# Kernel optimization log

Hardware: AMD Instinct MI355X
Metric: run time of the kernel (lower is better)

The kernel has to match this reference:

```python
import jax, jax.numpy as jnp
import numpy as np

X_DIM = 512
Z_DIM = 16
HEADS = 8
DIM_HEAD = 64
INNER = HEADS * DIM_HEAD
EPS = 1e-5


def _layernorm(t, g, b):
    mu = jnp.mean(t, axis=-1, keepdims=True)
    var = jnp.mean(jnp.square(t - mu), axis=-1, keepdims=True)
    return (t - mu) * jax.lax.rsqrt(var + EPS) * g + b


def setup_inputs() -> dict:
    key = jax.random.key(0)
    ks = jax.random.split(key, 8)
    B, N = 4, 2048
    s_x = 1.0 / np.sqrt(X_DIM)
    s_z = 1.0 / np.sqrt(Z_DIM)
    s_i = 1.0 / np.sqrt(INNER)
    return {
        "x": jax.random.normal(ks[0], (B, N, X_DIM), dtype=jnp.float32),
        "z": jax.random.normal(ks[1], (B, 1, Z_DIM), dtype=jnp.float32),
        "ln_x_g": jnp.ones((X_DIM,), jnp.float32),
        "ln_x_b": jnp.zeros((X_DIM,), jnp.float32),
        "ln_z_g": jnp.ones((Z_DIM,), jnp.float32),
        "ln_z_b": jnp.zeros((Z_DIM,), jnp.float32),
        "Wq": jax.random.normal(ks[2], (X_DIM, INNER), jnp.float32) * s_x,
        "Wk": jax.random.normal(ks[3], (X_DIM, INNER), jnp.float32) * s_x,
        "Wv": jax.random.normal(ks[4], (X_DIM, INNER), jnp.float32) * s_x,
        "Wz": jax.random.normal(ks[5], (Z_DIM, 2 * X_DIM), jnp.float32) * s_z,
        "Wo": jax.random.normal(ks[6], (INNER, X_DIM), jnp.float32) * s_i,
        "bo": jnp.zeros((X_DIM,), jnp.float32),
    }


def reference(x, z, ln_x_g, ln_x_b, ln_z_g, ln_z_b, Wq, Wk, Wv, Wz, Wo, bo):
    scale = DIM_HEAD ** (-0.5)
    # z path: LN -> Linear -> SiLU -> split into FiLM scale/shift
    zp = jax.nn.silu(_layernorm(z, ln_z_g, ln_z_b) @ Wz)  # [B, 1, 2*x_dim]
    z1, z2 = jnp.split(zp, 2, axis=-1)
    x_mod = _layernorm(x, ln_x_g, ln_x_b) * z1 + z2       # [B, N, x_dim]
    B, N, _ = x.shape

    def heads(t):  # [B, N, inner] -> [B, h, N, d]
        return t.reshape(B, N, HEADS, DIM_HEAD).transpose(0, 2, 1, 3)

    q = heads(x_mod @ Wq)
    k = heads(x_mod @ Wk)
    v = heads(x_mod @ Wv)
    sim = jnp.einsum('bhid,bhjd->bhij', q, k) * scale
    attn = jax.nn.softmax(sim, axis=-1)
    out = jnp.einsum('bhij,bhjd->bhid', attn, v)           # [B, h, N, d]
    out = out.transpose(0, 2, 1, 3).reshape(B, N, INNER)
    return out @ Wo + bo
```

## Files before the change

kernel.cpp:

```cpp
#include <hip/hip_runtime.h>

#define XD 512
#define HEADS 8
#define DH 64
#define NSEQ 2048
#define NBATCH 4
#define NROWS (NBATCH*NSEQ)

#define SCALE_L2E 0.18033688011112042f
#define DEFER_THR 4.0f

typedef __attribute__((ext_vector_type(8))) short bf16x8;
typedef __attribute__((ext_vector_type(8))) unsigned short u16x8;
typedef __attribute__((ext_vector_type(4))) float f32x4;
typedef __attribute__((ext_vector_type(16))) float f32x16;

__device__ __forceinline__ unsigned short f2bf(float f) {
  union { float f; unsigned u; } v; v.f = f;
  return (unsigned short)((v.u + 0x7fffu + ((v.u >> 16) & 1u)) >> 16);
}

__device__ __forceinline__ float fexp2(float x) {
#if __has_builtin(__builtin_amdgcn_exp2f)
  return __builtin_amdgcn_exp2f(x);
#else
  return exp2f(x);
#endif
}

__device__ __forceinline__ unsigned cvt_pk_bf16(float lo, float hi) {
  unsigned r;
  asm("v_cvt_pk_bf16_f32 %0, %1, %2" : "=v"(r) : "v"(lo), "v"(hi));
  return r;
}

__device__ __forceinline__ void gload_lds16(const unsigned short* g, unsigned short* l) {
  __builtin_amdgcn_global_load_lds(
      (const __attribute__((address_space(1))) unsigned int*)g,
      (__attribute__((address_space(3))) unsigned int*)l, 16, 0, 0);
}

__global__ __launch_bounds__(256) void zpath_kernel(
    const float* __restrict__ z, const float* __restrict__ g, const float* __restrict__ b,
    const float* __restrict__ Wz, float* __restrict__ z12) {
  int bb = blockIdx.x;
  int t = threadIdx.x;
  float zv[16];
  float mean = 0.f;
#pragma unroll
  for (int i = 0; i < 16; ++i) { zv[i] = z[bb * 16 + i]; mean += zv[i]; }
  mean *= (1.f / 16.f);
  float var = 0.f;
#pragma unroll
  for (int i = 0; i < 16; ++i) { float d = zv[i] - mean; var += d * d; }
  var *= (1.f / 16.f);
  float rs = rsqrtf(var + 1e-5f);
  float zn[16];
#pragma unroll
  for (int i = 0; i < 16; ++i) zn[i] = (zv[i] - mean) * rs * g[i] + b[i];
  for (int c = t; c < 1024; c += 256) {
    float acc = 0.f;
#pragma unroll
    for (int i = 0; i < 16; ++i) acc += zn[i] * Wz[i * 1024 + c];
    float s = acc / (1.f + __expf(-acc));
    z12[bb * 1024 + c] = s;
  }
}

__global__ __launch_bounds__(256) void xmod_kernel(
    const float* __restrict__ x, const float* __restrict__ g, const float* __restrict__ b,
    const float* __restrict__ z12, unsigned short* __restrict__ xm) {
  int wave = threadIdx.x >> 6, lane = threadIdx.x & 63;
  int row = blockIdx.x * 4 + wave;
  const float* xr = x + (size_t)row * XD;
  float4 v0 = ((const float4*)xr)[lane * 2];
  float4 v1 = ((const float4*)xr)[lane * 2 + 1];
  float vv[8] = {v0.x, v0.y, v0.z, v0.w, v1.x, v1.y, v1.z, v1.w};
  float sum = 0.f, sq = 0.f;
#pragma unroll
  for (int i = 0; i < 8; ++i) { sum += vv[i]; sq += vv[i] * vv[i]; }
#pragma unroll
  for (int o = 32; o; o >>= 1) { sum += __shfl_xor(sum, o); sq += __shfl_xor(sq, o); }
  float mean = sum * (1.f / 512.f);
  float var = sq * (1.f / 512.f) - mean * mean;
  float rs = rsqrtf(var + 1e-5f);
  int bb = row >> 11;
  const float* zz = z12 + bb * 1024;
  int c0 = lane * 8;
  u16x8 o8;
#pragma unroll
  for (int i = 0; i < 8; ++i) {
    int c = c0 + i;
    float t = (vv[i] - mean) * rs * g[c] + b[c];
    t = t * zz[c] + zz[512 + c];
    o8[i] = f2bf(t);
  }
  *(u16x8*)(xm + (size_t)row * XD + c0) = o8;
}

__global__ __launch_bounds__(256) void wtrans4_kernel(
    const float* __restrict__ W0, const float* __restrict__ W1,
    const float* __restrict__ W2, const float* __restrict__ W3,
    unsigned short* __restrict__ dst) {
  int idx = blockIdx.x * 256 + threadIdx.x;
  int w = idx >> 18;
  int e = idx & 262143;
  int n = e >> 9, k = e & 511;
  const float* W = (w == 0) ? W0 : (w == 1) ? W1 : (w == 2) ? W2 : W3;
  dst[idx] = f2bf(W[k * 512 + n]);
}

__global__ __launch_bounds__(256, 2) void gemm_qkv_kernel(
    const unsigned short* __restrict__ A, const unsigned short* __restrict__ Wt,
    unsigned short* __restrict__ Qo, unsigned short* __restrict__ Ko,
    unsigned short* __restrict__ Vo) {
  __shared__ unsigned short Alds[128 * 64];
  __shared__ unsigned short Blds[128 * 64];
  int widx = threadIdx.x >> 6, lane = threadIdx.x & 63;
  int blk = blockIdx.x;
  int nt = blk % 12, mt = blk / 12;
  int blkM = mt * 128, blkN = nt * 128;
  int wr = widx >> 1, wc = widx & 1;
  int lr = lane & 15, lg = lane >> 4;
  int srow = lane >> 3, sc8 = lane & 7;

  f32x4 acc[4][4] = {};

  for (int kc = 0; kc < 512; kc += 64) {
#pragma unroll
    for (int i = 0; i < 4; ++i) {
      int rb = widx * 32 + i * 8;
      int row = rb + srow;
      int cs = (sc8 ^ (row & 7)) * 8;
      gload_lds16(A + (size_t)(blkM + row) * 512 + kc + cs, &Alds[rb * 64]);
      gload_lds16(Wt + (size_t)(blkN + row) * 512 + kc + cs, &Blds[rb * 64]);
    }
    __syncthreads();

#pragma unroll
    for (int kh = 0; kh < 2; ++kh) {
      bf16x8 bfr[4];
#pragma unroll
      for (int ni = 0; ni < 4; ++ni) {
        int brow = wc * 64 + ni * 16 + lr;
        bfr[ni] = *(const bf16x8*)&Blds[brow * 64 + (((kh * 4 + lg) ^ (brow & 7)) * 8)];
      }
#pragma unroll
      for (int mi = 0; mi < 4; ++mi) {
        int arow = wr * 64 + mi * 16 + lr;
        bf16x8 afr = *(const bf16x8*)&Alds[arow * 64 + (((kh * 4 + lg) ^ (arow & 7)) * 8)];
#pragma unroll
        for (int ni = 0; ni < 4; ++ni)
          acc[mi][ni] = __builtin_amdgcn_mfma_f32_16x16x32_bf16(afr, bfr[ni], acc[mi][ni], 0, 0, 0);
      }
    }
    __syncthreads();
  }

  int cg = blkN >> 9;
#pragma unroll
  for (int mi = 0; mi < 4; ++mi)
#pragma unroll
    for (int ni = 0; ni < 4; ++ni) {
      int col = blkN + wc * 64 + ni * 16 + lr;
      int c = col & 511;
#pragma unroll
      for (int j = 0; j < 4; ++j) {
        int row = blkM + wr * 64 + mi * 16 + lg * 4 + j;
        float v = acc[mi][ni][j];
        if (cg == 0) {
          Qo[(size_t)row * 512 + c] = f2bf(v * SCALE_L2E);
        } else if (cg == 1) {
          Ko[(size_t)row * 512 + c] = f2bf(v);
        } else {
          int bb = row >> 11, n = row & 2047, h = c >> 6, d = c & 63;
          int j4 = n & 15;
          int slot = (j4 & 3) | (((j4 >> 3) & 1) << 2) | (((j4 >> 2) & 1) << 3);
          int np = (n & ~15) | slot;
          Vo[(((size_t)(bb * HEADS + h) * DH + d) << 11) + np] = f2bf(v);
        }
      }
    }
}

__global__ __launch_bounds__(256, 2) void gemm_out_kernel(
    const unsigned short* __restrict__ A, const unsigned short* __restrict__ Wt,
    float* __restrict__ out, const float* __restrict__ bias) {
  __shared__ unsigned short Alds[128 * 64];
  __shared__ unsigned short Blds[64 * 64];
  int widx = threadIdx.x >> 6, lane = threadIdx.x & 63;
  int blk = blockIdx.x;
  int nt = blk & 7, mt = blk >> 3;
  int blkM = mt * 128, blkN = nt * 64;
  int wr = widx >> 1, wc = widx & 1;
  int lr = lane & 15, lg = lane >> 4;
  int srow = lane >> 3, sc8 = lane & 7;

  f32x4 acc[4][2] = {};

  for (int kc = 0; kc < 512; kc += 64) {
#pragma unroll
    for (int i = 0; i < 4; ++i) {
      int rb = widx * 32 + i * 8;
      int row = rb + srow;
      int cs = (sc8 ^ (row & 7)) * 8;
      gload_lds16(A + (size_t)(blkM + row) * 512 + kc + cs, &Alds[rb * 64]);
    }
#pragma unroll
    for (int i = 0; i < 2; ++i) {
      int rb = widx * 16 + i * 8;
      int row = rb + srow;
      int cs = (sc8 ^ (row & 7)) * 8;
      gload_lds16(Wt + (size_t)(blkN + row) * 512 + kc + cs, &Blds[rb * 64]);
    }
    __syncthreads();

#pragma unroll
    for (int kh = 0; kh < 2; ++kh) {
      bf16x8 bfr[2];
#pragma unroll
      for (int ni = 0; ni < 2; ++ni) {
        int brow = wc * 32 + ni * 16 + lr;
        bfr[ni] = *(const bf16x8*)&Blds[brow * 64 + (((kh * 4 + lg) ^ (brow & 7)) * 8)];
      }
#pragma unroll
      for (int mi = 0; mi < 4; ++mi) {
        int arow = wr * 64 + mi * 16 + lr;
        bf16x8 afr = *(const bf16x8*)&Alds[arow * 64 + (((kh * 4 + lg) ^ (arow & 7)) * 8)];
#pragma unroll
        for (int ni = 0; ni < 2; ++ni)
          acc[mi][ni] = __builtin_amdgcn_mfma_f32_16x16x32_bf16(afr, bfr[ni], acc[mi][ni], 0, 0, 0);
      }
    }
    __syncthreads();
  }

#pragma unroll
  for (int mi = 0; mi < 4; ++mi)
#pragma unroll
    for (int ni = 0; ni < 2; ++ni) {
      int col = blkN + wc * 32 + ni * 16 + lr;
#pragma unroll
      for (int j = 0; j < 4; ++j) {
        int row = blkM + wr * 64 + mi * 16 + lg * 4 + j;
        out[(size_t)row * 512 + col] = acc[mi][ni][j] + bias[col];
      }
    }
}


#define KVCHUNK 128
#define NCHUNK (NSEQ / KVCHUNK)

#define STAGE(buf, kcc) do {                                              \
    _Pragma("unroll")                                                     \
    for (int i = 0; i < 4; ++i) {                                         \
      int rbk = widx * 32 + i * 8;                                        \
      int rowk = rbk + (lane >> 3);                                       \
      int csk = (lane & 7) ^ (rowk & 7);                                  \
      gload_lds16(Kg + (size_t)((kcc) + rowk) * 512 + csk * 8, &Klds[buf][rbk * 64]); \
      int rbv = widx * 16 + i * 4;                                        \
      int rowv = rbv + (lane >> 4);                                       \
      int csv = (lane & 15) ^ (rowv & 15);                                \
      gload_lds16(Vg + (size_t)rowv * NSEQ + (kcc) + csv * 8, &Vlds[buf][rbv * 128]); \
    }                                                                     \
  } while (0)

#define PROCESS_LDS64(kb_, vb_, half) do {                                \
    f32x16 s[2];                                                          \
    __builtin_amdgcn_s_setprio(1);                                        \
    _Pragma("unroll")                                                     \
    for (int kt = 0; kt < 2; ++kt) {                                      \
      int krow = (half) * 64 + kt * 32 + ql;                              \
      f32x16 z = {};                                                      \
      _Pragma("unroll")                                                   \
      for (int ks = 0; ks < 4; ++ks) {                                    \
        bf16x8 kf = *(const bf16x8*)((kb_) + krow * 64 + (((ks * 2 + hi) ^ (krow & 7)) * 8)); \
        z = __builtin_amdgcn_mfma_f32_32x32x16_bf16(kf, qf[ks], z, 0, 0, 0); \
      }                                                                   \
      s[kt] = z;                                                          \
    }                                                                     \
    __builtin_amdgcn_s_setprio(0);                                        \
    float m8 = s[0][0];                                                   \
    _Pragma("unroll")                                                     \
    for (int i = 1; i < 16; ++i) m8 = fmaxf(m8, s[0][i]);                 \
    _Pragma("unroll")                                                     \
    for (int i = 0; i < 16; ++i) m8 = fmaxf(m8, s[1][i]);                 \
    m8 = fmaxf(m8, __shfl_xor(m8, 32));                                   \
    bool grow = (m8 > m0 + DEFER_THR);                                    \
    if (__any((int)grow)) {                                               \
      float mn = fmaxf(m0, m8);                                           \
      float al = fexp2(m0 - mn);                                          \
      m0 = mn; l0 *= al;                                                  \
      _Pragma("unroll")                                                   \
      for (int dt = 0; dt < 2; ++dt)                                      \
        _Pragma("unroll")                                                 \
        for (int j = 0; j < 16; ++j) o[dt][j] *= al;                      \
    }                                                                     \
    float p0[16], p1[16]; float rs = 0.f;                                 \
    _Pragma("unroll")                                                     \
    for (int i = 0; i < 16; ++i) { p0[i] = fexp2(s[0][i] - m0); rs += p0[i]; } \
    _Pragma("unroll")                                                     \
    for (int i = 0; i < 16; ++i) { p1[i] = fexp2(s[1][i] - m0); rs += p1[i]; } \
    rs += __shfl_xor(rs, 32);                                             \
    l0 += rs;                                                             \
    union { unsigned w[4]; bf16x8 v; } pf[4];                             \
    _Pragma("unroll")                                                     \
    for (int d2 = 0; d2 < 4; ++d2) {                                      \
      pf[0].w[d2] = cvt_pk_bf16(p0[2 * d2], p0[2 * d2 + 1]);              \
      pf[1].w[d2] = cvt_pk_bf16(p0[8 + 2 * d2], p0[8 + 2 * d2 + 1]);      \
      pf[2].w[d2] = cvt_pk_bf16(p1[2 * d2], p1[2 * d2 + 1]);              \
      pf[3].w[d2] = cvt_pk_bf16(p1[8 + 2 * d2], p1[8 + 2 * d2 + 1]);      \
    }                                                                     \
    __builtin_amdgcn_s_setprio(1);                                        \
    _Pragma("unroll")                                                     \
    for (int dt = 0; dt < 2; ++dt) {                                      \
      int vrow = dt * 32 + ql;                                            \
      f32x16 acc = o[dt];                                                 \
      _Pragma("unroll")                                                   \
      for (int g = 0; g < 4; ++g) {                                       \
        int sv = (half) * 8 + g * 2 + hi;                                 \
        bf16x8 vf = *(const bf16x8*)((vb_) + vrow * 128 + ((sv ^ (vrow & 15)) * 8)); \
        acc = __builtin_amdgcn_mfma_f32_32x32x16_bf16(vf, pf[g].v, acc, 0, 0, 0); \
      }                                                                   \
      o[dt] = acc;                                                        \
    }                                                                     \
    __builtin_amdgcn_s_setprio(0);                                        \
  } while (0)

__global__ __launch_bounds__(256, 2) void attn_kernel(
    const unsigned short* __restrict__ Q, const unsigned short* __restrict__ K,
    const unsigned short* __restrict__ VT, unsigned short* __restrict__ O) {
  __shared__ unsigned short Klds[2][128 * 64];
  __shared__ unsigned short Vlds[2][64 * 128];
  int widx = threadIdx.x >> 6, lane = threadIdx.x & 63;
  int blk = blockIdx.x;
  int xcd = blk & 7;
  int idx = blk >> 3;
  int bh = xcd * 4 + (idx >> 4);
  int qg = idx & 15;
  int b = bh >> 3, h = bh & 7;
  int ql = lane & 31, hi = lane >> 5;
  int qrow0 = qg * 128 + widx * 32;

  bf16x8 qf[4];
  const unsigned short* Qp = Q + (size_t)(b * NSEQ + qrow0 + ql) * 512 + h * 64 + hi * 8;
#pragma unroll
  for (int ks = 0; ks < 4; ++ks) qf[ks] = *(const bf16x8*)(Qp + ks * 16);

  const unsigned short* Kg = K + (size_t)b * NSEQ * 512 + h * 64;
  const unsigned short* Vg = VT + (size_t)bh * DH * NSEQ;

  float m0 = -3.0e38f, l0 = 0.f;
  f32x16 o[2] = {};

  STAGE(0, 0);
  __syncthreads();
  int cur = 0;
  for (int t = 0; t < NCHUNK; ++t) {
    if (t + 1 < NCHUNK) STAGE(cur ^ 1, (t + 1) * KVCHUNK);
    const unsigned short* kb_ = &Klds[cur][0];
    const unsigned short* vb_ = &Vlds[cur][0];
    PROCESS_LDS64(kb_, vb_, 0);
    PROCESS_LDS64(kb_, vb_, 1);
    __syncthreads();
    cur ^= 1;
  }

  {
    float inv = 1.f / l0;
    size_t rowb = (size_t)(b * NSEQ + qrow0 + ql) * 512 + h * 64 + hi * 4;
#pragma unroll
    for (int dt = 0; dt < 2; ++dt)
#pragma unroll
      for (int c = 0; c < 8; ++c) {
        unsigned w = cvt_pk_bf16(o[dt][2 * c] * inv, o[dt][2 * c + 1] * inv);
        int d0 = dt * 32 + 8 * (c >> 1) + (c & 1) * 2;
        *(unsigned*)(O + rowb + d0) = w;
      }
  }
}

extern "C" void kernel_launch(void* const* d_in, const int* in_sizes, int n_in,
                              void* d_out, int out_size, void* d_ws, size_t ws_size,
                              hipStream_t stream) {
  const float* x   = (const float*)d_in[0];
  const float* z   = (const float*)d_in[1];
  const float* lxg = (const float*)d_in[2];
  const float* lxb = (const float*)d_in[3];
  const float* lzg = (const float*)d_in[4];
  const float* lzb = (const float*)d_in[5];
  const float* Wq  = (const float*)d_in[6];
  const float* Wk  = (const float*)d_in[7];
  const float* Wv  = (const float*)d_in[8];
  const float* Wz  = (const float*)d_in[9];
  const float* Wo  = (const float*)d_in[10];
  const float* bo  = (const float*)d_in[11];

  char* ws = (char*)d_ws;
  unsigned short* xm  = (unsigned short*)(ws);
  unsigned short* qb  = (unsigned short*)(ws + 8388608);
  unsigned short* kb  = (unsigned short*)(ws + 16777216);
  unsigned short* vt  = (unsigned short*)(ws + 25165824);
  unsigned short* ao  = (unsigned short*)(ws + 33554432);
  unsigned short* wqt = (unsigned short*)(ws + 41943040);
  unsigned short* wot = (unsigned short*)(ws + 43515904);
  float*          z12 = (float*)(ws + 44040192);

  zpath_kernel<<<NBATCH, 256, 0, stream>>>(z, lzg, lzb, Wz, z12);
  xmod_kernel<<<NROWS / 4, 256, 0, stream>>>(x, lxg, lxb, z12, xm);
  wtrans4_kernel<<<4096, 256, 0, stream>>>(Wq, Wk, Wv, Wo, wqt);
  gemm_qkv_kernel<<<768, 256, 0, stream>>>(xm, wqt, qb, kb, vt);
  attn_kernel<<<512, 256, 0, stream>>>(qb, kb, vt, ao);
  gemm_out_kernel<<<512, 256, 0, stream>>>(ao, wot, (float*)d_out, bo);
}
```

Measured before the change: 111.4 us.

## Split attention KV range across two wave groups and tile weight transpose via LDS

The attention kernel now runs 512 threads per block, with two groups of four waves each handling half of the key/value sequence (split-K flash attention). Each group keeps its own online-softmax state, and the two partial results are merged through LDS at the end. This doubles the waves per query block to raise latency hiding and occupancy, at the cost of an extra LDS merge and smaller 64-row KV chunks. Separately, the weight transpose kernel uses a 32x32 shared-memory tile so that both its global reads and writes are coalesced.

Result: faster. 106.0 us (-4.9%).

```diff
diff --git a/kernel.cpp b/kernel.cpp
--- a/kernel.cpp
+++ b/kernel.cpp
@@ -102,12 +102,21 @@
     const float* __restrict__ W0, const float* __restrict__ W1,
     const float* __restrict__ W2, const float* __restrict__ W3,
     unsigned short* __restrict__ dst) {
-  int idx = blockIdx.x * 256 + threadIdx.x;
-  int w = idx >> 18;
-  int e = idx & 262143;
-  int n = e >> 9, k = e & 511;
+  __shared__ float tile[32][33];
+  int blk = blockIdx.x;
+  int w = blk >> 8;
+  int t = blk & 255;
+  int tn = t >> 4, tk = t & 15;
   const float* W = (w == 0) ? W0 : (w == 1) ? W1 : (w == 2) ? W2 : W3;
-  dst[idx] = f2bf(W[k * 512 + n]);
+  int r = threadIdx.x >> 5, c = threadIdx.x & 31;
+#pragma unroll
+  for (int i = 0; i < 4; ++i)
+    tile[r + 8 * i][c] = W[(size_t)(tk * 32 + r + 8 * i) * 512 + tn * 32 + c];
+  __syncthreads();
+  unsigned short* d = dst + (size_t)w * 262144;
+#pragma unroll
+  for (int i = 0; i < 4; ++i)
+    d[(size_t)(tn * 32 + r + 8 * i) * 512 + tk * 32 + c] = f2bf(tile[c][r + 8 * i]);
 }
 
 __global__ __launch_bounds__(256, 2) void gemm_qkv_kernel(
@@ -249,29 +258,26 @@
 }
 
 
-#define KVCHUNK 128
-#define NCHUNK (NSEQ / KVCHUNK)
-
-#define STAGE(buf, kcc) do {                                              \
-    _Pragma("unroll")                                                     \
-    for (int i = 0; i < 4; ++i) {                                         \
-      int rbk = widx * 32 + i * 8;                                        \
-      int rowk = rbk + (lane >> 3);                                       \
-      int csk = (lane & 7) ^ (rowk & 7);                                  \
-      gload_lds16(Kg + (size_t)((kcc) + rowk) * 512 + csk * 8, &Klds[buf][rbk * 64]); \
-      int rbv = widx * 16 + i * 4;                                        \
-      int rowv = rbv + (lane >> 4);                                       \
-      int csv = (lane & 15) ^ (rowv & 15);                                \
-      gload_lds16(Vg + (size_t)rowv * NSEQ + (kcc) + csv * 8, &Vlds[buf][rbv * 128]); \
+#define AKV 64
+#define NCH_S 16
+
+#define STAGE_S(s_, buf, kcc) do {                                        \
+    _Pragma("unroll")                                                     \
+    for (int i = 0; i < 2; ++i) {                                         \
+      int rb = wq * 16 + i * 8;                                           \
+      int row = rb + (lane >> 3);                                         \
+      int cs = (lane & 7) ^ (row & 7);                                    \
+      gload_lds16(Kg + (size_t)((kcc) + row) * 512 + cs * 8, KLDS(s_, buf) + rb * 64); \
+      gload_lds16(Vg + (size_t)row * NSEQ + (kcc) + cs * 8, VLDS(s_, buf) + rb * 64);  \
     }                                                                     \
   } while (0)
 
-#define PROCESS_LDS64(kb_, vb_, half) do {                                \
+#define PROCESS64(kb_, vb_) do {                                          \
     f32x16 s[2];                                                          \
     __builtin_amdgcn_s_setprio(1);                                        \
     _Pragma("unroll")                                                     \
     for (int kt = 0; kt < 2; ++kt) {                                      \
-      int krow = (half) * 64 + kt * 32 + ql;                              \
+      int krow = kt * 32 + ql;                                            \
       f32x16 z = {};                                                      \
       _Pragma("unroll")                                                   \
       for (int ks = 0; ks < 4; ++ks) {                                    \
@@ -319,8 +325,7 @@
       f32x16 acc = o[dt];                                                 \
       _Pragma("unroll")                                                   \
       for (int g = 0; g < 4; ++g) {                                       \
-        int sv = (half) * 8 + g * 2 + hi;                                 \
-        bf16x8 vf = *(const bf16x8*)((vb_) + vrow * 128 + ((sv ^ (vrow & 15)) * 8)); \
+        bf16x8 vf = *(const bf16x8*)((vb_) + vrow * 64 + (((g * 2 + hi) ^ (vrow & 7)) * 8)); \
         acc = __builtin_amdgcn_mfma_f32_32x32x16_bf16(vf, pf[g].v, acc, 0, 0, 0); \
       }                                                                   \
       o[dt] = acc;                                                        \
@@ -328,12 +333,16 @@
     __builtin_amdgcn_s_setprio(0);                                        \
   } while (0)
 
-__global__ __launch_bounds__(256, 2) void attn_kernel(
+__global__ __launch_bounds__(512, 4) void attn_kernel(
     const unsigned short* __restrict__ Q, const unsigned short* __restrict__ K,
     const unsigned short* __restrict__ VT, unsigned short* __restrict__ O) {
-  __shared__ unsigned short Klds[2][128 * 64];
-  __shared__ unsigned short Vlds[2][64 * 128];
-  int widx = threadIdx.x >> 6, lane = threadIdx.x & 63;
+  __shared__ __align__(16) unsigned short SH[2][2][2][64 * 64];
+#define KLDS(s_, bf) (&SH[0][s_][bf][0])
+#define VLDS(s_, bf) (&SH[1][s_][bf][0])
+  int tid = threadIdx.x;
+  int widx = tid >> 6, lane = tid & 63;
+  int strm = widx >> 2;
+  int wq = widx & 3;
   int blk = blockIdx.x;
   int xcd = blk & 7;
   int idx = blk >> 3;
@@ -341,40 +350,55 @@
   int qg = idx & 15;
   int b = bh >> 3, h = bh & 7;
   int ql = lane & 31, hi = lane >> 5;
-  int qrow0 = qg * 128 + widx * 32;
+  int qrow0 = qg * 128 + wq * 32;
 
   bf16x8 qf[4];
   const unsigned short* Qp = Q + (size_t)(b * NSEQ + qrow0 + ql) * 512 + h * 64 + hi * 8;
 #pragma unroll
   for (int ks = 0; ks < 4; ++ks) qf[ks] = *(const bf16x8*)(Qp + ks * 16);
 
-  const unsigned short* Kg = K + (size_t)b * NSEQ * 512 + h * 64;
-  const unsigned short* Vg = VT + (size_t)bh * DH * NSEQ;
+  const unsigned short* Kg = K + (size_t)b * NSEQ * 512 + h * 64 + (size_t)strm * 1024 * 512;
+  const unsigned short* Vg = VT + (size_t)bh * DH * NSEQ + strm * 1024;
 
   float m0 = -3.0e38f, l0 = 0.f;
   f32x16 o[2] = {};
 
-  STAGE(0, 0);
+  STAGE_S(strm, 0, 0);
   __syncthreads();
   int cur = 0;
-  for (int t = 0; t < NCHUNK; ++t) {
-    if (t + 1 < NCHUNK) STAGE(cur ^ 1, (t + 1) * KVCHUNK);
-    const unsigned short* kb_ = &Klds[cur][0];
-    const unsigned short* vb_ = &Vlds[cur][0];
-    PROCESS_LDS64(kb_, vb_, 0);
-    PROCESS_LDS64(kb_, vb_, 1);
+  for (int t = 0; t < NCH_S; ++t) {
+    if (t + 1 < NCH_S) STAGE_S(strm, cur ^ 1, (t + 1) * AKV);
+    const unsigned short* kb_ = KLDS(strm, cur);
+    const unsigned short* vb_ = VLDS(strm, cur);
+    PROCESS64(kb_, vb_);
     __syncthreads();
     cur ^= 1;
   }
 
-  {
-    float inv = 1.f / l0;
+  float* sm = (float*)&SH[0][0][0][0];
+  if (strm == 1) {
+    int base = (wq * 64 + lane) * 34;
+    sm[base] = m0;
+    sm[base + 1] = l0;
+#pragma unroll
+    for (int j = 0; j < 16; ++j) { sm[base + 2 + j] = o[0][j]; sm[base + 18 + j] = o[1][j]; }
+  }
+  __syncthreads();
+  if (strm == 0) {
+    int base = (wq * 64 + lane) * 34;
+    float mB = sm[base], lB = sm[base + 1];
+    float mN = fmaxf(m0, mB);
+    float aA = fexp2(m0 - mN), aB = fexp2(mB - mN);
+    float inv = 1.f / (l0 * aA + lB * aB);
+    float aAi = aA * inv, aBi = aB * inv;
     size_t rowb = (size_t)(b * NSEQ + qrow0 + ql) * 512 + h * 64 + hi * 4;
 #pragma unroll
     for (int dt = 0; dt < 2; ++dt)
 #pragma unroll
       for (int c = 0; c < 8; ++c) {
-        unsigned w = cvt_pk_bf16(o[dt][2 * c] * inv, o[dt][2 * c + 1] * inv);
+        float vlo = o[dt][2 * c] * aAi + sm[base + 2 + dt * 16 + 2 * c] * aBi;
+        float vhi = o[dt][2 * c + 1] * aAi + sm[base + 2 + dt * 16 + 2 * c + 1] * aBi;
+        unsigned w = cvt_pk_bf16(vlo, vhi);
         int d0 = dt * 32 + 8 * (c >> 1) + (c & 1) * 2;
         *(unsigned*)(O + rowb + d0) = w;
       }
@@ -409,8 +433,8 @@
 
   zpath_kernel<<<NBATCH, 256, 0, stream>>>(z, lzg, lzb, Wz, z12);
   xmod_kernel<<<NROWS / 4, 256, 0, stream>>>(x, lxg, lxb, z12, xm);
-  wtrans4_kernel<<<4096, 256, 0, stream>>>(Wq, Wk, Wv, Wo, wqt);
+  wtrans4_kernel<<<1024, 256, 0, stream>>>(Wq, Wk, Wv, Wo, wqt);
   gemm_qkv_kernel<<<768, 256, 0, stream>>>(xm, wqt, qb, kb, vt);
-  attn_kernel<<<512, 256, 0, stream>>>(qb, kb, vt, ao);
+  attn_kernel<<<512, 512, 0, stream>>>(qb, kb, vt, ao);
   gemm_out_kernel<<<512, 256, 0, stream>>>(ao, wot, (float*)d_out, bo);
 }
```
